# Kernel optimization log

Hardware: AMD Instinct MI355X
Metric: run time of the kernel (lower is better)

The kernel has to match this reference:

```python
import jax, jax.numpy as jnp
import numpy as np

EPS = 1e-12  # F.normalize eps

def _l2norm(v):
    n = jnp.sqrt(jnp.sum(v * v, axis=-1, keepdims=True))
    return v / jnp.maximum(n, EPS)

def setup_inputs() -> dict:
    key = jax.random.key(0)
    k1, k2, k3 = jax.random.split(key, 3)
    B, C, H, Wd = 32, 256, 64, 64
    M = 64
    x = jax.random.normal(k1, (B, C, H, Wd), dtype=jnp.float32)
    stdv = 1.0 / np.sqrt(M)
    W = jax.random.uniform(k2, (M, C), dtype=jnp.float32, minval=-stdv, maxval=stdv)
    label_batch = jax.random.randint(k3, (B,), 0, 2)
    return {"x": x, "W": W, "label_batch": label_batch}

def reference(x, W, label_batch):
    B, C, H, Wd = x.shape
    M = W.shape[0]
    # [B, HW, C] tokens; key == query == flattened input (pos=False)
    tok = x.transpose(0, 2, 3, 1).reshape(B, H * Wd, C)
    # per-pixel contribution to each prototype, softmax over pixels (dim=1)
    proto_weight = jax.nn.softmax(jnp.einsum('bnc,mc->bnm', tok, W), axis=1)
    # prototypes [B, M, C], L2-normalized
    proto = _l2norm(jnp.einsum('bnm,bnc->bmc', proto_weight, tok))
    # relevance of each pixel to each prototype, softmax over prototypes
    score = jax.nn.softmax(jnp.einsum('bnc,bmc->bnm', tok, proto), axis=-1)
    # reconstructed query
    new_query = _l2norm(jnp.einsum('bnm,bmc->bnc', score, proto))
    # compact loss: MSE(keys, nearest prototype) (new_cpt == 'True')
    top1 = jnp.argmax(score, axis=-1)                      # [B, HW]
    pos = jnp.take_along_axis(proto, top1[:, :, None], axis=1)  # [B, HW, C]
    compact_loss = jnp.mean((tok - pos) ** 2)
    # distance loss: push prototypes apart
    p2 = jnp.sum(proto * proto, axis=-1)                   # [B, M]
    sqd = p2[:, :, None] + p2[:, None, :] - 2.0 * jnp.einsum('bmc,bkc->bmk', proto, proto)
    dis = 1.0 - sqd
    dis = dis * (dis > 0).astype(dis.dtype)
    dis = jnp.triu(dis, k=1)
    dis_loss = jnp.mean(jnp.sum(dis, axis=(1, 2)) * 2.0 / (M * (M - 1)))
    out = new_query.transpose(0, 2, 1).reshape(B, C, H, Wd)
    return (out, compact_loss, dis_loss)
```

## Files before the change

kernel.cpp:

```cpp
#include <hip/hip_runtime.h>
#include <math.h>

#define B 32
#define C 256
#define M 64
#define N 4096

typedef __attribute__((ext_vector_type(8))) short s16x8;
typedef __attribute__((ext_vector_type(8))) __bf16 bf16x8;
typedef __attribute__((ext_vector_type(4))) __bf16 bf16x4;
typedef __attribute__((ext_vector_type(4))) float f32x4;
typedef __attribute__((ext_vector_type(4))) unsigned short u16x4;
typedef __attribute__((ext_vector_type(8))) unsigned short u16x8;

static constexpr float EPS = 1e-12f;

__device__ __forceinline__ unsigned short b16(float f) {
    __bf16 h = (__bf16)f;
    return __builtin_bit_cast(unsigned short, h);
}
__device__ __forceinline__ float bf2f(unsigned short h) {
    return __uint_as_float((unsigned)h << 16);
}
__device__ __forceinline__ f32x4 MFMA(s16x8 a, s16x8 b, f32x4 c) {
    return __builtin_amdgcn_mfma_f32_16x16x32_bf16(
        __builtin_bit_cast(bf16x8, a), __builtin_bit_cast(bf16x8, b), c, 0, 0, 0);
}
__device__ __forceinline__ s16x8 cvt8(const f32x4 a, const f32x4 b) {
    bf16x8 h;
    h[0] = (__bf16)a[0]; h[1] = (__bf16)a[1]; h[2] = (__bf16)a[2]; h[3] = (__bf16)a[3];
    h[4] = (__bf16)b[0]; h[5] = (__bf16)b[1]; h[6] = (__bf16)b[2]; h[7] = (__bf16)b[3];
    return __builtin_bit_cast(s16x8, h);
}
__device__ __forceinline__ int swz(int n) {
    return (((n >> 2) & 3) | ((n & 1) << 2)) << 3;
}

__global__ __launch_bounds__(256) void k01(const float* __restrict__ x,
                                           const float* __restrict__ Wf,
                                           unsigned short* __restrict__ xbt,
                                           unsigned short* __restrict__ Sb,
                                           float* __restrict__ xsq) {
    const int nb = blockIdx.x, b = blockIdx.y;
    const int t = threadIdx.x;
    __shared__ unsigned short tsT[64 * 256];
    __shared__ float xred[16][68];
    const int nq = t & 15, cq = t >> 4;
    float part[4] = {0.f, 0.f, 0.f, 0.f};
    const float* xrow = x + (size_t)b * C * N + (size_t)nb * 64 + 4 * nq;
#pragma unroll
    for (int step = 0; step < 4; ++step) {
        const int c0 = cq * 4 + step * 64;
        f32x4 q[4];
#pragma unroll
        for (int i = 0; i < 4; ++i) q[i] = *(const f32x4*)(xrow + (size_t)(c0 + i) * N);
#pragma unroll
        for (int k = 0; k < 4; ++k) {
            const int n = 4 * nq + k;
            bf16x4 hb;
#pragma unroll
            for (int i = 0; i < 4; ++i) {
                part[k] += q[i][k] * q[i][k];
                hb[i] = (__bf16)q[i][k];
            }
            *(u16x4*)(&tsT[n * 256 + (c0 ^ swz(n))]) = __builtin_bit_cast(u16x4, hb);
        }
    }
#pragma unroll
    for (int k = 0; k < 4; ++k) xred[cq][4 * nq + k] = part[k];
    __syncthreads();
    if (t < 64) {
        float s = 0.f;
#pragma unroll
        for (int j = 0; j < 16; ++j) s += xred[j][t];
        xsq[(size_t)b * N + nb * 64 + t] = s;
    }
    {
        const int l = t & 31, nh = t >> 5;
#pragma unroll
        for (int j = 0; j < 8; ++j) {
            const int n = nh + 8 * j;
            const int c0 = l * 8;
            const u16x8 v = *(const u16x8*)(&tsT[n * 256 + (c0 ^ swz(n))]);
            *(u16x8*)(xbt + ((size_t)b * N + nb * 64 + n) * C + c0) = v;
        }
    }
    const int wv = t >> 6, lane = t & 63, li = lane & 15, lk = lane >> 4;
    const f32x4 zv = {0.f, 0.f, 0.f, 0.f};
    f32x4 acc[4] = {zv, zv, zv, zv};
    const float* wr = Wf + (size_t)(wv * 16 + li) * C + lk * 8;
#pragma unroll
    for (int c0 = 0; c0 < C; c0 += 32) {
        const s16x8 bfrag = cvt8(*(const f32x4*)(wr + c0), *(const f32x4*)(wr + c0 + 4));
#pragma unroll
        for (int s = 0; s < 4; ++s) {
            const int n = s * 16 + li;
            const s16x8 a = *(const s16x8*)(&tsT[n * 256 + ((lk * 8 + c0) ^ swz(n))]);
            acc[s] = MFMA(a, bfrag, acc[s]);
        }
    }
    unsigned short* Srow = Sb + ((size_t)b * M + wv * 16 + li) * N + nb * 64;
#pragma unroll
    for (int s = 0; s < 4; ++s) {
        bf16x4 h;
#pragma unroll
        for (int r = 0; r < 4; ++r) h[r] = (__bf16)acc[s][r];
        *(u16x4*)(Srow + s * 16 + lk * 4) = __builtin_bit_cast(u16x4, h);
    }
}

__global__ __launch_bounds__(256) void k2_softmax_n(const unsigned short* __restrict__ Sb,
                                                    unsigned short* __restrict__ Pb) {
    const int m = blockIdx.x, b = blockIdx.y;
    const unsigned short* col = Sb + ((size_t)b * M + m) * N;
    unsigned short* po = Pb + ((size_t)b * M + m) * N;
    const int t = threadIdx.x;
    float v[16];
    const u16x8 h0 = *(const u16x8*)(col + t * 16);
    const u16x8 h1 = *(const u16x8*)(col + t * 16 + 8);
#pragma unroll
    for (int i = 0; i < 8; ++i) v[i] = bf2f(h0[i]);
#pragma unroll
    for (int i = 0; i < 8; ++i) v[8 + i] = bf2f(h1[i]);
    float mx = -INFINITY;
#pragma unroll
    for (int i = 0; i < 16; ++i) mx = fmaxf(mx, v[i]);
#pragma unroll
    for (int off = 32; off >= 1; off >>= 1) mx = fmaxf(mx, __shfl_xor(mx, off));
    __shared__ float redm[4], reds[4];
    const int wave = t >> 6, lane = t & 63;
    if (lane == 0) redm[wave] = mx;
    __syncthreads();
    mx = fmaxf(fmaxf(redm[0], redm[1]), fmaxf(redm[2], redm[3]));
    float s = 0.f;
#pragma unroll
    for (int i = 0; i < 16; ++i) {
        v[i] = __expf(v[i] - mx);
        s += v[i];
    }
#pragma unroll
    for (int off = 32; off >= 1; off >>= 1) s += __shfl_xor(s, off);
    if (lane == 0) reds[wave] = s;
    __syncthreads();
    s = reds[0] + reds[1] + reds[2] + reds[3];
    const float inv = 1.f / s;
    bf16x8 o0, o1;
#pragma unroll
    for (int i = 0; i < 8; ++i) o0[i] = (__bf16)(v[i] * inv);
#pragma unroll
    for (int i = 0; i < 8; ++i) o1[i] = (__bf16)(v[8 + i] * inv);
    *(u16x8*)(po + t * 16) = __builtin_bit_cast(u16x8, o0);
    *(u16x8*)(po + t * 16 + 8) = __builtin_bit_cast(u16x8, o1);
}

__global__ __launch_bounds__(256) void k3_mfma(const float* __restrict__ x,
                                               const unsigned short* __restrict__ Pb,
                                               float* __restrict__ parts) {
    const int ck = blockIdx.x, b = blockIdx.y;
    const int wv = threadIdx.x >> 6, lane = threadIdx.x & 63;
    const int li = lane & 15, lk = lane >> 4;
    const int c0w = wv * 64;
    const int nb = ck * 512;
    const f32x4 zv = {0.f, 0.f, 0.f, 0.f};
    f32x4 acc[4][4];
#pragma unroll
    for (int s = 0; s < 4; ++s)
#pragma unroll
        for (int u = 0; u < 4; ++u) acc[s][u] = zv;
    const float* ar = x + ((size_t)b * C + c0w + li) * N + nb + lk * 8;
    const unsigned short* br = Pb + ((size_t)b * M + li) * N + nb + lk * 8;
#pragma unroll 4
    for (int n0 = 0; n0 < 512; n0 += 32) {
        s16x8 af[4], bf_[4];
#pragma unroll
        for (int s = 0; s < 4; ++s) {
            const float* p = ar + (size_t)(s * 16) * N + n0;
            af[s] = cvt8(*(const f32x4*)p, *(const f32x4*)(p + 4));
        }
#pragma unroll
        for (int u = 0; u < 4; ++u) bf_[u] = *(const s16x8*)(br + (size_t)(u * 16) * N + n0);
#pragma unroll
        for (int s = 0; s < 4; ++s)
#pragma unroll
            for (int u = 0; u < 4; ++u) acc[s][u] = MFMA(af[s], bf_[u], acc[s][u]);
    }
    float* pp = parts + ((size_t)b * 8 + ck) * M * C;
#pragma unroll
    for (int s = 0; s < 4; ++s)
#pragma unroll
        for (int u = 0; u < 4; ++u)
            *(f32x4*)(pp + (size_t)(u * 16 + li) * C + c0w + s * 16 + lk * 4) = acc[s][u];
}

__global__ __launch_bounds__(256) void k3b_reduce(const float* __restrict__ parts,
                                                  unsigned short* __restrict__ proto_bf,
                                                  unsigned short* __restrict__ protoT_bf,
                                                  float* __restrict__ p2) {
    const int mb = blockIdx.x, b = blockIdx.y;
    const int t = threadIdx.x;
    const int ml = t >> 5, cl = t & 31;
    const int m = mb * 8 + ml;
    const int c0 = cl * 8;
    float v[8] = {0.f, 0.f, 0.f, 0.f, 0.f, 0.f, 0.f, 0.f};
    const float* pbase = parts + (size_t)b * 8 * M * C + (size_t)m * C + c0;
#pragma unroll
    for (int ck = 0; ck < 8; ++ck) {
        const f32x4 q0 = *(const f32x4*)(pbase + (size_t)ck * M * C);
        const f32x4 q1 = *(const f32x4*)(pbase + (size_t)ck * M * C + 4);
#pragma unroll
        for (int j = 0; j < 4; ++j) { v[j] += q0[j]; v[4 + j] += q1[j]; }
    }
    float sq = 0.f;
#pragma unroll
    for (int j = 0; j < 8; ++j) sq += v[j] * v[j];
#pragma unroll
    for (int off = 16; off >= 1; off >>= 1) sq += __shfl_xor(sq, off);
    const float denom = fmaxf(sqrtf(sq), EPS);
    const float scale = 1.f / denom;
    if (cl == 0) p2[b * M + m] = sq / (denom * denom);
    bf16x8 h;
#pragma unroll
    for (int j = 0; j < 8; ++j) h[j] = (__bf16)(v[j] * scale);
    const u16x8 hu = __builtin_bit_cast(u16x8, h);
    *(u16x8*)(proto_bf + ((size_t)b * M + m) * C + c0) = hu;
#pragma unroll
    for (int j = 0; j < 8; ++j)
        protoT_bf[((size_t)b * C + c0 + j) * M + m] = hu[j];
}

__global__ __launch_bounds__(256) void k4_score(const unsigned short* __restrict__ proto_bf,
                                                const unsigned short* __restrict__ xbt,
                                                const float* __restrict__ p2,
                                                const float* __restrict__ xsq,
                                                unsigned short* __restrict__ pnm,
                                                float* __restrict__ cparts) {
    const int b = blockIdx.y;
    const int wv = threadIdx.x >> 6, lane = threadIdx.x & 63;
    const int li = lane & 15, lk = lane >> 4;
    const int nbase = blockIdx.x * 256 + wv * 64;
    const f32x4 zv = {0.f, 0.f, 0.f, 0.f};
    f32x4 acc[4][4];
#pragma unroll
    for (int s = 0; s < 4; ++s)
#pragma unroll
        for (int u = 0; u < 4; ++u) acc[s][u] = zv;
    const unsigned short* ar = proto_bf + ((size_t)b * M + li) * C + lk * 8;
    const unsigned short* br = xbt + ((size_t)b * N + nbase + li) * C + lk * 8;
#pragma unroll
    for (int c0 = 0; c0 < C; c0 += 32) {
        s16x8 af[4], bf_[4];
#pragma unroll
        for (int s = 0; s < 4; ++s) af[s] = *(const s16x8*)(ar + (size_t)(s * 16) * C + c0);
#pragma unroll
        for (int u = 0; u < 4; ++u) bf_[u] = *(const s16x8*)(br + (size_t)(u * 16) * C + c0);
#pragma unroll
        for (int s = 0; s < 4; ++s)
#pragma unroll
            for (int u = 0; u < 4; ++u) acc[s][u] = MFMA(af[s], bf_[u], acc[s][u]);
    }
    float csum = 0.f;
#pragma unroll
    for (int u = 0; u < 4; ++u) {
        const int n = nbase + u * 16 + li;
        float vmax = -INFINITY;
#pragma unroll
        for (int s = 0; s < 4; ++s)
#pragma unroll
            for (int r = 0; r < 4; ++r) vmax = fmaxf(vmax, acc[s][u][r]);
        vmax = fmaxf(vmax, __shfl_xor(vmax, 16));
        vmax = fmaxf(vmax, __shfl_xor(vmax, 32));
        int t1 = 1 << 30;
#pragma unroll
        for (int s = 0; s < 4; ++s)
#pragma unroll
            for (int r = 0; r < 4; ++r)
                if (acc[s][u][r] == vmax) t1 = min(t1, s * 16 + lk * 4 + r);
        t1 = min(t1, __shfl_xor(t1, 16));
        t1 = min(t1, __shfl_xor(t1, 32));
        unsigned short* prow = pnm + ((size_t)b * N + n) * M;
#pragma unroll
        for (int s = 0; s < 4; ++s) {
            bf16x4 h;
#pragma unroll
            for (int r = 0; r < 4; ++r) h[r] = (__bf16)__expf(acc[s][u][r] - vmax);
            *(u16x4*)(prow + s * 16 + lk * 4) = __builtin_bit_cast(u16x4, h);
        }
        if (lk == 0) csum += xsq[(size_t)b * N + n] - 2.f * vmax + p2[b * M + t1];
    }
#pragma unroll
    for (int off = 32; off >= 1; off >>= 1) csum += __shfl_xor(csum, off);
    __shared__ float red[4];
    if (lane == 0) red[wv] = csum;
    __syncthreads();
    if (threadIdx.x == 0)
        cparts[b * 16 + blockIdx.x] = red[0] + red[1] + red[2] + red[3];
}

__global__ __launch_bounds__(256) void k4b_mfma(const unsigned short* __restrict__ pnm,
                                                const unsigned short* __restrict__ protoT_bf,
                                                float* __restrict__ out) {
    const int b = blockIdx.y;
    const int wv = threadIdx.x >> 6, lane = threadIdx.x & 63;
    const int li = lane & 15, lk = lane >> 4;
    const int n0 = blockIdx.x * 64;
    const int cb = wv * 64;
    const f32x4 zv = {0.f, 0.f, 0.f, 0.f};
    f32x4 acc[4][4];
#pragma unroll
    for (int s = 0; s < 4; ++s)
#pragma unroll
        for (int u = 0; u < 4; ++u) acc[s][u] = zv;
    const unsigned short* ar = pnm + ((size_t)b * N + n0 + li) * M + lk * 8;
    const unsigned short* br = protoT_bf + ((size_t)b * C + cb + li) * M + lk * 8;
#pragma unroll
    for (int m0 = 0; m0 < M; m0 += 32) {
        s16x8 af[4], bf_[4];
#pragma unroll
        for (int s = 0; s < 4; ++s) af[s] = *(const s16x8*)(ar + (size_t)(s * 16) * M + m0);
#pragma unroll
        for (int u = 0; u < 4; ++u) bf_[u] = *(const s16x8*)(br + (size_t)(u * 16) * M + m0);
#pragma unroll
        for (int s = 0; s < 4; ++s)
#pragma unroll
            for (int u = 0; u < 4; ++u) acc[s][u] = MFMA(af[s], bf_[u], acc[s][u]);
    }
    __shared__ float ls[4][64];
    __shared__ float ls2[64];
    float psq[4][4];
#pragma unroll
    for (int s = 0; s < 4; ++s)
#pragma unroll
        for (int r = 0; r < 4; ++r) {
            float sum = 0.f;
#pragma unroll
            for (int u = 0; u < 4; ++u) sum += acc[s][u][r] * acc[s][u][r];
#pragma unroll
            for (int off = 8; off >= 1; off >>= 1) sum += __shfl_xor(sum, off);
            psq[s][r] = sum;
        }
    if (li == 0) {
#pragma unroll
        for (int s = 0; s < 4; ++s)
#pragma unroll
            for (int r = 0; r < 4; ++r) ls[wv][s * 16 + lk * 4 + r] = psq[s][r];
    }
    __syncthreads();
    if (threadIdx.x < 64) {
        const int tt = threadIdx.x;
        const float tot = ls[0][tt] + ls[1][tt] + ls[2][tt] + ls[3][tt];
        ls2[tt] = 1.f / fmaxf(sqrtf(tot), EPS);
    }
    __syncthreads();
    float scl[4][4];
#pragma unroll
    for (int s = 0; s < 4; ++s)
#pragma unroll
        for (int r = 0; r < 4; ++r) scl[s][r] = ls2[s * 16 + lk * 4 + r];
    float* ob = out + (size_t)b * C * N;
#pragma unroll
    for (int s = 0; s < 4; ++s)
#pragma unroll
        for (int u = 0; u < 4; ++u) {
            f32x4 q;
#pragma unroll
            for (int r = 0; r < 4; ++r) q[r] = acc[s][u][r] * scl[s][r];
            *(f32x4*)(ob + (size_t)(cb + u * 16 + li) * N + n0 + s * 16 + lk * 4) = q;
        }
}

__global__ __launch_bounds__(256) void k5_dis(const unsigned short* __restrict__ proto_bf,
                                              const float* __restrict__ p2,
                                              float* __restrict__ dparts) {
    const int q = blockIdx.x;
    const int b = blockIdx.y;
    const unsigned short* pr = proto_bf + (size_t)b * M * C;
    __shared__ float pl[M * C];
    for (int idx = threadIdx.x; idx < M * C; idx += 256) {
        int m = idx >> 8, c = idx & 255;
        pl[m * 256 + (c ^ (m & 31))] = bf2f(pr[idx]);
    }
    __syncthreads();
    float sum = 0.f;
    for (int k = 0; k < 2; ++k) {
        const int pair = q * 512 + k * 256 + threadIdx.x;
        const int i = pair >> 6, j = pair & 63;
        if (j > i) {
            float g = 0.f;
#pragma unroll 8
            for (int c = 0; c < C; ++c)
                g += pl[i * 256 + (c ^ (i & 31))] * pl[j * 256 + (c ^ (j & 31))];
            const float d = 1.f - (p2[b * M + i] + p2[b * M + j] - 2.f * g);
            sum += fmaxf(d, 0.f);
        }
    }
#pragma unroll
    for (int off = 32; off >= 1; off >>= 1) sum += __shfl_xor(sum, off);
    __shared__ float red[4];
    const int wave = threadIdx.x >> 6, lane = threadIdx.x & 63;
    if (lane == 0) red[wave] = sum;
    __syncthreads();
    if (threadIdx.x == 0) dparts[b * 8 + q] = red[0] + red[1] + red[2] + red[3];
}

__global__ __launch_bounds__(256) void k6_final(const float* __restrict__ cparts, int ncp,
                                                const float* __restrict__ dparts,
                                                float* __restrict__ losses) {
    const int t = threadIdx.x;
    float cs = 0.f;
    for (int i = t; i < ncp; i += 256) cs += cparts[i];
    float ds = dparts[t];
#pragma unroll
    for (int off = 32; off >= 1; off >>= 1) {
        cs += __shfl_xor(cs, off);
        ds += __shfl_xor(ds, off);
    }
    __shared__ float rc[4], rd[4];
    const int wave = t >> 6, lane = t & 63;
    if (lane == 0) { rc[wave] = cs; rd[wave] = ds; }
    __syncthreads();
    if (t == 0) {
        const float ctot = rc[0] + rc[1] + rc[2] + rc[3];
        const float dtot = rd[0] + rd[1] + rd[2] + rd[3];
        losses[0] = ctot / ((float)B * (float)N * (float)C);
        losses[1] = dtot * (2.f / (float)(M * (M - 1))) / (float)B;
    }
}

extern "C" void kernel_launch(void* const* d_in, const int* in_sizes, int n_in,
                              void* d_out, int out_size, void* d_ws, size_t ws_size,
                              hipStream_t stream) {
    const float* x = (const float*)d_in[0];
    const float* Wf = (const float*)d_in[1];
    float* out = (float*)d_out;
    float* wsf = (float*)d_ws;
    float* losses = out + (size_t)B * C * N;

    unsigned short* xbt = (unsigned short*)d_out;
    unsigned short* Sbf = (unsigned short*)wsf;
    float* parts = wsf;
    unsigned short* Pbf = (unsigned short*)(wsf + 4194304);
    unsigned short* pnm = Pbf;
    float* xsq = wsf + 8388608;
    unsigned short* proto_bf = (unsigned short*)(wsf + 8519680);
    unsigned short* protoT_bf = (unsigned short*)(wsf + 8781824);
    float* p2 = wsf + 9052160;
    float* cparts = wsf + 9054208;
    float* dparts = wsf + 9054720;

    k01<<<dim3(N / 64, B), 256, 0, stream>>>(x, Wf, xbt, Sbf, xsq);
    k2_softmax_n<<<dim3(M, B), 256, 0, stream>>>(Sbf, Pbf);
    k3_mfma<<<dim3(8, B), 256, 0, stream>>>(x, Pbf, parts);
    k3b_reduce<<<dim3(8, B), 256, 0, stream>>>(parts, proto_bf, protoT_bf, p2);
    k4_score<<<dim3(N / 256, B), 256, 0, stream>>>(proto_bf, xbt, p2, xsq, pnm, cparts);
    k4b_mfma<<<dim3(N / 64, B), 256, 0, stream>>>(pnm, protoT_bf, out);
    k5_dis<<<dim3(8, B), 256, 0, stream>>>(proto_bf, p2, dparts);
    k6_final<<<1, 256, 0, stream>>>(cparts, B * 16, dparts, losses);
}
```

Before: 173.4 us.

## Halve k01 pixel tile to 32, hoist all x loads, shuffle-reduce norms

The first kernel now handles 32 pixels per block instead of 64, which doubles the grid and halves its LDS tile. Each thread issues all eight of its global loads up front for more memory-level parallelism. The squared-norm reduction uses wave shuffles instead of a large shared-memory table, and the LDS swizzle is replaced by a simpler one. In the MFMA stage each wave now covers 16 pixels by 32 prototypes, so W fragments are reloaded per pixel tile, adding some W traffic and redundant bf16 conversions.

New measurement: 205.8 us. 18.7% more time.

```diff
diff --git a/kernel.cpp b/kernel.cpp
--- a/kernel.cpp
+++ b/kernel.cpp
@@ -15,10 +15,6 @@
 
 static constexpr float EPS = 1e-12f;
 
-__device__ __forceinline__ unsigned short b16(float f) {
-    __bf16 h = (__bf16)f;
-    return __builtin_bit_cast(unsigned short, h);
-}
 __device__ __forceinline__ float bf2f(unsigned short h) {
     return __uint_as_float((unsigned)h << 16);
 }
@@ -32,8 +28,8 @@
     h[4] = (__bf16)b[0]; h[5] = (__bf16)b[1]; h[6] = (__bf16)b[2]; h[7] = (__bf16)b[3];
     return __builtin_bit_cast(s16x8, h);
 }
-__device__ __forceinline__ int swz(int n) {
-    return (((n >> 2) & 3) | ((n & 1) << 2)) << 3;
+__device__ __forceinline__ int fsw(int n) {
+    return ((n >> 2) & 3) << 4;
 }
 
 __global__ __launch_bounds__(256) void k01(const float* __restrict__ x,
@@ -43,69 +39,79 @@
                                            float* __restrict__ xsq) {
     const int nb = blockIdx.x, b = blockIdx.y;
     const int t = threadIdx.x;
-    __shared__ unsigned short tsT[64 * 256];
-    __shared__ float xred[16][68];
-    const int nq = t & 15, cq = t >> 4;
+    __shared__ unsigned short tsT[32 * 256];
+    __shared__ float red[4][32];
+    const int wave = t >> 6, lane = t & 63;
+    const int nq = t & 7, cp = t >> 3;
+    const float* xrow = x + (size_t)b * C * N + (size_t)nb * 32 + 4 * nq;
+    f32x4 q[8];
+#pragma unroll
+    for (int step = 0; step < 2; ++step)
+#pragma unroll
+        for (int i = 0; i < 4; ++i)
+            q[step * 4 + i] = *(const f32x4*)(xrow + (size_t)(cp * 4 + step * 128 + i) * N);
     float part[4] = {0.f, 0.f, 0.f, 0.f};
-    const float* xrow = x + (size_t)b * C * N + (size_t)nb * 64 + 4 * nq;
-#pragma unroll
-    for (int step = 0; step < 4; ++step) {
-        const int c0 = cq * 4 + step * 64;
-        f32x4 q[4];
-#pragma unroll
-        for (int i = 0; i < 4; ++i) q[i] = *(const f32x4*)(xrow + (size_t)(c0 + i) * N);
+#pragma unroll
+    for (int step = 0; step < 2; ++step) {
+        const int c0 = cp * 4 + step * 128;
 #pragma unroll
         for (int k = 0; k < 4; ++k) {
             const int n = 4 * nq + k;
             bf16x4 hb;
 #pragma unroll
             for (int i = 0; i < 4; ++i) {
-                part[k] += q[i][k] * q[i][k];
-                hb[i] = (__bf16)q[i][k];
+                part[k] += q[step * 4 + i][k] * q[step * 4 + i][k];
+                hb[i] = (__bf16)q[step * 4 + i][k];
             }
-            *(u16x4*)(&tsT[n * 256 + (c0 ^ swz(n))]) = __builtin_bit_cast(u16x4, hb);
-        }
-    }
-#pragma unroll
-    for (int k = 0; k < 4; ++k) xred[cq][4 * nq + k] = part[k];
-    __syncthreads();
-    if (t < 64) {
-        float s = 0.f;
-#pragma unroll
-        for (int j = 0; j < 16; ++j) s += xred[j][t];
-        xsq[(size_t)b * N + nb * 64 + t] = s;
-    }
+            *(u16x4*)(&tsT[n * 256 + (c0 ^ fsw(n))]) = __builtin_bit_cast(u16x4, hb);
+        }
+    }
+#pragma unroll
+    for (int k = 0; k < 4; ++k) {
+        part[k] += __shfl_xor(part[k], 8);
+        part[k] += __shfl_xor(part[k], 16);
+        part[k] += __shfl_xor(part[k], 32);
+    }
+    if (lane < 8) {
+#pragma unroll
+        for (int k = 0; k < 4; ++k) red[wave][4 * lane + k] = part[k];
+    }
+    __syncthreads();
+    if (t < 32)
+        xsq[(size_t)b * N + nb * 32 + t] =
+            red[0][t] + red[1][t] + red[2][t] + red[3][t];
     {
-        const int l = t & 31, nh = t >> 5;
-#pragma unroll
-        for (int j = 0; j < 8; ++j) {
-            const int n = nh + 8 * j;
+        const int l = t & 31, r = t >> 5;
+#pragma unroll
+        for (int j = 0; j < 4; ++j) {
+            const int n = r + 8 * j;
             const int c0 = l * 8;
-            const u16x8 v = *(const u16x8*)(&tsT[n * 256 + (c0 ^ swz(n))]);
-            *(u16x8*)(xbt + ((size_t)b * N + nb * 64 + n) * C + c0) = v;
-        }
-    }
-    const int wv = t >> 6, lane = t & 63, li = lane & 15, lk = lane >> 4;
+            const u16x8 v = *(const u16x8*)(&tsT[n * 256 + (c0 ^ fsw(n))]);
+            *(u16x8*)(xbt + ((size_t)b * N + nb * 32 + n) * C + c0) = v;
+        }
+    }
+    const int li = lane & 15, lk = lane >> 4;
+    const int s = wave >> 1, mh = (wave & 1) * 32;
     const f32x4 zv = {0.f, 0.f, 0.f, 0.f};
-    f32x4 acc[4] = {zv, zv, zv, zv};
-    const float* wr = Wf + (size_t)(wv * 16 + li) * C + lk * 8;
+    f32x4 acc[2] = {zv, zv};
+    const int an = s * 16 + li;
 #pragma unroll
     for (int c0 = 0; c0 < C; c0 += 32) {
-        const s16x8 bfrag = cvt8(*(const f32x4*)(wr + c0), *(const f32x4*)(wr + c0 + 4));
-#pragma unroll
-        for (int s = 0; s < 4; ++s) {
-            const int n = s * 16 + li;
-            const s16x8 a = *(const s16x8*)(&tsT[n * 256 + ((lk * 8 + c0) ^ swz(n))]);
-            acc[s] = MFMA(a, bfrag, acc[s]);
-        }
-    }
-    unsigned short* Srow = Sb + ((size_t)b * M + wv * 16 + li) * N + nb * 64;
-#pragma unroll
-    for (int s = 0; s < 4; ++s) {
+        const s16x8 a = *(const s16x8*)(&tsT[an * 256 + ((lk * 8 + c0) ^ fsw(an))]);
+#pragma unroll
+        for (int u = 0; u < 2; ++u) {
+            const float* wr = Wf + (size_t)(mh + u * 16 + li) * C + c0 + lk * 8;
+            const s16x8 bf_ = cvt8(*(const f32x4*)wr, *(const f32x4*)(wr + 4));
+            acc[u] = MFMA(a, bf_, acc[u]);
+        }
+    }
+#pragma unroll
+    for (int u = 0; u < 2; ++u) {
         bf16x4 h;
 #pragma unroll
-        for (int r = 0; r < 4; ++r) h[r] = (__bf16)acc[s][r];
-        *(u16x4*)(Srow + s * 16 + lk * 4) = __builtin_bit_cast(u16x4, h);
+        for (int r = 0; r < 4; ++r) h[r] = (__bf16)acc[u][r];
+        *(u16x4*)(Sb + ((size_t)b * M + mh + u * 16 + li) * N + nb * 32 + s * 16 + lk * 4) =
+            __builtin_bit_cast(u16x4, h);
     }
 }
 
@@ -447,7 +453,7 @@
     float* cparts = wsf + 9054208;
     float* dparts = wsf + 9054720;
 
-    k01<<<dim3(N / 64, B), 256, 0, stream>>>(x, Wf, xbt, Sbf, xsq);
+    k01<<<dim3(N / 32, B), 256, 0, stream>>>(x, Wf, xbt, Sbf, xsq);
     k2_softmax_n<<<dim3(M, B), 256, 0, stream>>>(Sbf, Pbf);
     k3_mfma<<<dim3(8, B), 256, 0, stream>>>(x, Pbf, parts);
     k3b_reduce<<<dim3(8, B), 256, 0, stream>>>(parts, proto_bf, protoT_bf, p2);
```
